# Kernel optimization log

Hardware: AMD Instinct MI355X
Metric: run time of the kernel (lower is better)

## Reference

```python
import jax, jax.numpy as jnp
import numpy as np

J, L = 4, 8
M = N = 128
B = 2
EPS = 1e-6  # abs_eps smoothing: |z|_eps = sqrt(re^2 + im^2 + eps)


def indices_third_order(J, L):
    # For each bandpass filter i = j1*L + l1, pair with every filter of scale
    # j2 >= j1 (all L angles) plus the lowpass (index J*L).
    # Count = J*L*(L*(J+1)/2 + 1) == num_coefficients.
    i_list, j_list = [], []
    for j1 in range(J):
        for l1 in range(L):
            i = j1 * L + l1
            for j2 in range(j1, J):
                for l2 in range(L):
                    i_list.append(i)
                    j_list.append(j2 * L + l2)
            i_list.append(i)
            j_list.append(J * L)
    return np.asarray(i_list), np.asarray(j_list)


def make_filters(J, L, M, N):
    # Real frequency-domain Morlet-like Gaussian bumps at J scales x L angles,
    # plus one lowpass. Shape (1, J*L+1, M, N), float32.
    kx = 2.0 * np.pi * np.fft.fftfreq(M)[:, None]
    ky = 2.0 * np.pi * np.fft.fftfreq(N)[None, :]
    filts = []
    for j in range(J):
        k0 = 0.8 * np.pi / 2.0 ** j
        sigma = 0.5 * k0
        for l in range(L):
            theta = np.pi * l / L
            cx, cy = k0 * np.cos(theta), k0 * np.sin(theta)
            filts.append(np.exp(-((kx - cx) ** 2 + (ky - cy) ** 2) / (2.0 * sigma ** 2)))
    sigma_lp = 0.8 * np.pi / 2.0 ** J
    filts.append(np.exp(-(kx ** 2 + ky ** 2) / (2.0 * sigma_lp ** 2)))
    return np.stack(filts)[None].astype(np.float32)


def abs_eps(z):
    return jnp.sqrt(z.real ** 2 + z.imag ** 2 + EPS)


def setup_inputs() -> dict:
    key = jax.random.key(0)
    x = jax.random.normal(key, (B, 1, M, N), dtype=jnp.float32)
    filters = jnp.asarray(make_filters(J, L, M, N))  # (1, 33, M, N)
    return {"x": x, "filters": filters}


def reference(x, filters):
    idx0, idx1 = indices_third_order(J, L)
    # first-order filtering: (B, nf, M, N) complex
    xf = jnp.fft.ifft2(filters * jnp.fft.fft2(x))
    xa = abs_eps(xf)  # real (B, nf, M, N)
    # cross-scale correlation: (B, nf_i, nf_j, M, N)
    inner = jnp.fft.ifft2(filters[:, None] * jnp.fft.fft2(xa)[:, :, None])
    out = jnp.real(jnp.conj(xf)[:, None] * inner).mean(axis=(-2, -1))  # (B, nf, nf)
    return out[:, idx0, idx1]  # (B, 672)
```

## Files before the change

kernel.cpp:

```cpp
#include <hip/hip_runtime.h>
#include <math.h>


#define PI_F 3.14159265358979323846f

__device__ __forceinline__ void make_tw(int lane, float* twr, float* twi) {
#pragma unroll
  for (int s = 0; s < 6; ++s) {
    int h = 32 >> s;
    float ang = -PI_F * (float)(lane & (h - 1)) / (float)h;
    float sv, cv;
    __sincosf(ang, &sv, &cv);
    twr[s] = cv; twi[s] = sv;
  }
  float ang = -PI_F * (float)lane / 64.0f;
  float sv, cv;
  __sincosf(ang, &sv, &cv);
  twr[6] = cv; twi[6] = sv;
}

template <int S>
__device__ __forceinline__ void fft128_dif(float& ar, float& ai, float& br, float& bi,
                                           const float* twr, const float* twi, int lane) {
  float s6r = twr[6], s6i = (S > 0) ? twi[6] : -twi[6];
  float ur = ar + br, ui = ai + bi;
  float vr = ar - br, vi = ai - bi;
  ar = ur; ai = ui;
  br = vr * s6r - vi * s6i;
  bi = vr * s6i + vi * s6r;
#pragma unroll
  for (int s = 0; s < 6; ++s) {
    int h = 32 >> s;
    float wr = twr[s], wi = (S > 0) ? twi[s] : -twi[s];
    bool hi = (lane & h) != 0;
    float pr, pi2;
    pr = __shfl_xor(ar, h, 64); pi2 = __shfl_xor(ai, h, 64);
    if (!hi) { ar += pr; ai += pi2; }
    else { float dr = pr - ar, di = pi2 - ai; ar = dr * wr - di * wi; ai = dr * wi + di * wr; }
    pr = __shfl_xor(br, h, 64); pi2 = __shfl_xor(bi, h, 64);
    if (!hi) { br += pr; bi += pi2; }
    else { float dr = pr - br, di = pi2 - bi; br = dr * wr - di * wi; bi = dr * wi + di * wr; }
  }
}

template <int NC>
__device__ __forceinline__ void transpose_r2c_n(float (&dr)[16], float (&di)[16],
    float (&er)[NC], float (&ei)[NC], float (&fr)[NC], float (&fi2)[NC],
    float2 (*tile)[128], int lane, int w, int colbase) {
#pragma unroll
  for (int ch = 0; ch < 2; ++ch) {
    if ((w >> 3) == ch) {
#pragma unroll
      for (int t = 0; t < 8; ++t) {
        int r = w * 8 + t;
        int rr = r & 63, sw = r & 15;
        tile[rr][lane ^ sw] = make_float2(dr[2 * t], di[2 * t]);
        tile[rr][(lane + 64) ^ sw] = make_float2(dr[2 * t + 1], di[2 * t + 1]);
      }
    }
    __syncthreads();
    {
      int sw = lane & 15;
#pragma unroll
      for (int ci = 0; ci < NC; ++ci) {
        int c = colbase + w * NC + ci;
        float2 v = tile[lane][c ^ sw];
        if (ch == 0) { er[ci] = v.x; ei[ci] = v.y; }
        else { fr[ci] = v.x; fi2[ci] = v.y; }
      }
    }
    __syncthreads();
  }
}

__global__ __launch_bounds__(1024, 2) void k_prep(const float* __restrict__ x,
    float2* __restrict__ X, float* __restrict__ out, const float* __restrict__ F,
    float* __restrict__ G) {
  __shared__ float2 tile[64][128];
  int tid = threadIdx.x;
  int bx = blockIdx.x;
  if (bx == 8) {
    if (tid < 1344) out[tid] = 0.f;
    return;
  }
  if (bx >= 9) {
    int j = bx - 9;
    const float* Fj = F + j * 16384;
    float* Gj = G + j * 16384;
    for (int k = tid; k < 16384; k += 1024) {
      int u = k >> 7, v = k & 127;
      int un = (128 - u) & 127, vn = (128 - v) & 127;
      float f = Fj[k], fn = Fj[un * 128 + vn];
      Gj[k] = 0.5f * (f * f + fn * fn);
    }
    return;
  }
  int b = bx >> 2, quarter = bx & 3;
  int lane = tid & 63, w = tid >> 6;
  float twr[7], twi[7]; make_tw(lane, twr, twi);
  const float* xb = x + b * 16384;
  float dr[16], di[16];
  float er[2], ei[2], fr[2], fi2[2];
#pragma unroll
  for (int t = 0; t < 8; ++t) {
    int r = w * 8 + t;
    float ar = xb[r * 128 + lane], ai2 = 0.f, br = xb[r * 128 + lane + 64], bi = 0.f;
    fft128_dif<1>(ar, ai2, br, bi, twr, twi, lane);
    dr[2 * t] = ar; di[2 * t] = ai2; dr[2 * t + 1] = br; di[2 * t + 1] = bi;
  }
  transpose_r2c_n<2>(dr, di, er, ei, fr, fi2, tile, lane, w, quarter * 32);
  int u0 = __brev((unsigned)lane) >> 25;
#pragma unroll
  for (int ci = 0; ci < 2; ++ci) {
    int c = quarter * 32 + w * 2 + ci;
    float ar = er[ci], ai2 = ei[ci], br = fr[ci], bi = fi2[ci];
    fft128_dif<1>(ar, ai2, br, bi, twr, twi, lane);
    int vn = __brev((unsigned)c) >> 25;
    X[b * 16384 + u0 * 128 + vn] = make_float2(ar, ai2);
    X[b * 16384 + (u0 + 1) * 128 + vn] = make_float2(br, bi);
  }
}

__global__ __launch_bounds__(1024, 2) void k_fields(const float2* __restrict__ X,
    const float* __restrict__ F, const float* __restrict__ G,
    float* __restrict__ dfld, float* __restrict__ xa) {
  __shared__ float2 tile[64][128];
  int tid = threadIdx.x, lane = tid & 63, w = tid >> 6;
  int bx = blockIdx.x;
  bool isd = (bx < 68);
  int b, half;
  bool has1 = false;
  const float* g0 = nullptr; const float* g1 = nullptr; const float* Fb = nullptr;
  float* o0; float* o1 = nullptr;
  if (isd) {
    int dp = bx >> 1; half = bx & 1;
    b = dp / 17; int p = dp - b * 17;
    int j0 = 2 * p; has1 = (p < 16);
    g0 = G + j0 * 16384;
    g1 = G + (j0 + 1) * 16384;
    o0 = dfld + (b * 33 + j0) * 16384;
    o1 = dfld + (b * 33 + j0 + 1) * 16384;
  } else {
    int q = bx - 68; int qi = q >> 1; half = q & 1;
    b = qi >> 5; int f = qi & 31;
    Fb = F + f * 16384;
    o0 = xa + qi * 16384;
  }
  float twr[7], twi[7]; make_tw(lane, twr, twi);
  const float2* Xb = X + b * 16384;
  float dr[16], di[16];
  float er[4], ei[4], fr[4], fi2[4];

#pragma unroll
  for (int t = 0; t < 8; ++t) {
    int r = w * 8 + t;
    float2 x0 = Xb[r * 128 + lane];
    float2 x1 = Xb[r * 128 + lane + 64];
    float ar, ai2, br, bi;
    if (isd) {
      float ga = g0[r * 128 + lane];
      float gb = has1 ? g1[r * 128 + lane] : 0.f;
      float gc = g0[r * 128 + lane + 64];
      float gd = has1 ? g1[r * 128 + lane + 64] : 0.f;
      ar = x0.x * ga - x0.y * gb; ai2 = x0.y * ga + x0.x * gb;
      br = x1.x * gc - x1.y * gd; bi = x1.y * gc + x1.x * gd;
    } else {
      float f0 = Fb[r * 128 + lane], f1 = Fb[r * 128 + lane + 64];
      ar = x0.x * f0; ai2 = x0.y * f0; br = x1.x * f1; bi = x1.y * f1;
    }
    fft128_dif<-1>(ar, ai2, br, bi, twr, twi, lane);
    dr[2 * t] = ar; di[2 * t] = ai2; dr[2 * t + 1] = br; di[2 * t + 1] = bi;
  }
  transpose_r2c_n<4>(dr, di, er, ei, fr, fi2, tile, lane, w, half * 64);

  const float sc = 1.0f / 16384.0f;
#pragma unroll
  for (int ci = 0; ci < 4; ++ci) {
    int c = half * 64 + w * 4 + ci;
    float ar = er[ci], ai2 = ei[ci], br = fr[ci], bi = fi2[ci];
    fft128_dif<-1>(ar, ai2, br, bi, twr, twi, lane);
    if (isd) {
      o0[c * 128 + lane] = ar;
      o0[c * 128 + lane + 64] = br;
      if (has1) {
        o1[c * 128 + lane] = ai2;
        o1[c * 128 + lane + 64] = bi;
      }
    } else {
      float t0r = ar * sc, t0i = ai2 * sc, t1r = br * sc, t1i = bi * sc;
      o0[c * 128 + lane] = sqrtf(t0r * t0r + t0i * t0i + 1e-6f);
      o0[c * 128 + lane + 64] = sqrtf(t1r * t1r + t1i * t1i + 1e-6f);
    }
  }
}

__global__ __launch_bounds__(512) void k_dot(const float* __restrict__ xa,
    const float* __restrict__ dfld, float* __restrict__ out) {
  int q = blockIdx.x;
  int im = q >> 3;
  int slice = (q >> 1) & 3;
  int jh = q & 1;
  int b = im >> 5, i = im & 31;
  int j0 = jh * 17;
  int t = threadIdx.x;
  const float4* xr = (const float4*)(xa + im * 16384 + slice * 4096);
  const float4* db = (const float4*)(dfld + (b * 33 + j0) * 16384 + slice * 4096);
  float acc[17];
#pragma unroll
  for (int j = 0; j < 17; ++j) acc[j] = 0.f;
#pragma unroll
  for (int it = 0; it < 2; ++it) {
    int k = it * 512 + t;
    float4 xv = xr[k];
#pragma unroll
    for (int j = 0; j < 17; ++j) {
      float4 dv = db[j * 4096 + k];
      acc[j] += xv.x * dv.x + xv.y * dv.y + xv.z * dv.z + xv.w * dv.w;
    }
  }
#pragma unroll
  for (int j = 0; j < 17; ++j) {
#pragma unroll
    for (int off = 32; off > 0; off >>= 1) acc[j] += __shfl_xor(acc[j], off, 64);
  }
  __shared__ float red[8][17];
  int w = t >> 6, lane = t & 63;
  if (lane == 0) {
#pragma unroll
    for (int j = 0; j < 17; ++j) red[w][j] = acc[j];
  }
  __syncthreads();
  if (t < 17) {
    int j = j0 + t;
    float s = 0.f;
#pragma unroll
    for (int w2 = 0; w2 < 8; ++w2) s += red[w2][t];
    int j1 = i >> 3, l1 = i & 7;
    const int pref[4] = {0, 264, 464, 600};
    int per = (4 - j1) * 8 + 1;
    int start = pref[j1] + l1 * per;
    int pos = -1;
    if (j == 32) pos = start + per - 1;
    else if (j < 32) {
      int j2 = j >> 3;
      if (j2 >= j1) pos = start + (j2 - j1) * 8 + (j & 7);
    }
    if (pos >= 0)
      atomicAdd(out + b * 672 + pos, s * (1.0f / 16384.0f) * (1.0f / 16384.0f));
  }
}

extern "C" void kernel_launch(void* const* d_in, const int* in_sizes, int n_in,
                              void* d_out, int out_size, void* d_ws, size_t ws_size,
                              hipStream_t stream) {
  (void)in_sizes; (void)n_in; (void)out_size; (void)ws_size;
  const float* x = (const float*)d_in[0];
  const float* F = (const float*)d_in[1];
  float* out = (float*)d_out;
  char* ws = (char*)d_ws;
  float2* X = (float2*)(ws + 0);
  float* dfld = (float*)(ws + 262144);
  float* xa = (float*)(ws + 4587520);
  float* G = (float*)(ws + 8781824);

  hipLaunchKernelGGL(k_prep, dim3(42), dim3(1024), 0, stream, x, X, out, F, G);
  hipLaunchKernelGGL(k_fields, dim3(196), dim3(1024), 0, stream, X, F, G, dfld, xa);
  hipLaunchKernelGGL(k_dot, dim3(512), dim3(512), 0, stream, xa, dfld, out);
}
```

Baseline: 103.3 us.

## Use half-wavefront 4-point FFT layout in k_fields and split G prep

Rewrites the k_fields 128-point FFTs so that each half-wavefront (32 lanes) handles one row with four elements per lane. The first two radix stages run in registers and only the remaining five use shuffles, which cuts cross-lane shuffle traffic and register-array size. The shared-memory transpose is rewritten to match the new layout and the launch bounds are relaxed to one block per SM. k_prep also splits the G-filter symmetrisation over four blocks per filter, raising the grid from 42 to 141 blocks for more parallelism.

```diff
diff --git a/kernel.cpp b/kernel.cpp
--- a/kernel.cpp
+++ b/kernel.cpp
@@ -73,6 +73,63 @@
   }
 }
 
+__device__ __forceinline__ void make_tw2(int q, float* t2r, float* t2i, float* hw) {
+#pragma unroll
+  for (int s = 0; s < 5; ++s) {
+    int h = 16 >> s;
+    float ang = -PI_F * (float)(q & (h - 1)) / (float)h;
+    float sv, cv;
+    __sincosf(ang, &sv, &cv);
+    t2r[s] = cv; t2i[s] = sv;
+  }
+  float sv, cv;
+  __sincosf(-PI_F * (float)q / 64.0f, &sv, &cv);         hw[0] = cv; hw[1] = sv;
+  __sincosf(-PI_F * (float)(q + 32) / 64.0f, &sv, &cv);  hw[2] = cv; hw[3] = sv;
+  __sincosf(-PI_F * (float)q / 32.0f, &sv, &cv);         hw[4] = cv; hw[5] = sv;
+}
+
+template <int S>
+__device__ __forceinline__ void fft128x2_dif(float (&cr)[4], float (&ci)[4],
+    const float* t2r, const float* t2i, const float* hw, int q) {
+  float T0r = hw[0], T0i = (S > 0) ? hw[1] : -hw[1];
+  float T1r = hw[2], T1i = (S > 0) ? hw[3] : -hw[3];
+  float T2r = hw[4], T2i = (S > 0) ? hw[5] : -hw[5];
+  {
+    float ur = cr[0] + cr[2], ui = ci[0] + ci[2];
+    float vr = cr[0] - cr[2], vi = ci[0] - ci[2];
+    cr[0] = ur; ci[0] = ui;
+    cr[2] = vr * T0r - vi * T0i; ci[2] = vr * T0i + vi * T0r;
+    ur = cr[1] + cr[3]; ui = ci[1] + ci[3];
+    vr = cr[1] - cr[3]; vi = ci[1] - ci[3];
+    cr[1] = ur; ci[1] = ui;
+    cr[3] = vr * T1r - vi * T1i; ci[3] = vr * T1i + vi * T1r;
+  }
+  {
+    float ur = cr[0] + cr[1], ui = ci[0] + ci[1];
+    float vr = cr[0] - cr[1], vi = ci[0] - ci[1];
+    cr[0] = ur; ci[0] = ui;
+    cr[1] = vr * T2r - vi * T2i; ci[1] = vr * T2i + vi * T2r;
+    ur = cr[2] + cr[3]; ui = ci[2] + ci[3];
+    vr = cr[2] - cr[3]; vi = ci[2] - ci[3];
+    cr[2] = ur; ci[2] = ui;
+    cr[3] = vr * T2r - vi * T2i; ci[3] = vr * T2i + vi * T2r;
+  }
+#pragma unroll
+  for (int s = 0; s < 5; ++s) {
+    int h = 16 >> s;
+    float wr = t2r[s], wi = (S > 0) ? t2i[s] : -t2i[s];
+    bool hi = (q & h) != 0;
+#pragma unroll
+    for (int m = 0; m < 4; ++m) {
+      float pr = __shfl_xor(cr[m], h, 64);
+      float pi2 = __shfl_xor(ci[m], h, 64);
+      if (!hi) { cr[m] += pr; ci[m] += pi2; }
+      else { float dr = pr - cr[m], di = pi2 - ci[m];
+             cr[m] = dr * wr - di * wi; ci[m] = dr * wi + di * wr; }
+    }
+  }
+}
+
 __global__ __launch_bounds__(1024, 2) void k_prep(const float* __restrict__ x,
     float2* __restrict__ X, float* __restrict__ out, const float* __restrict__ F,
     float* __restrict__ G) {
@@ -84,10 +141,13 @@
     return;
   }
   if (bx >= 9) {
-    int j = bx - 9;
+    int q = bx - 9;
+    int j = q >> 2, part = q & 3;
     const float* Fj = F + j * 16384;
     float* Gj = G + j * 16384;
-    for (int k = tid; k < 16384; k += 1024) {
+#pragma unroll
+    for (int it = 0; it < 4; ++it) {
+      int k = part * 4096 + it * 1024 + tid;
       int u = k >> 7, v = k & 127;
       int un = (128 - u) & 127, vn = (128 - v) & 127;
       float f = Fj[k], fn = Fj[un * 128 + vn];
@@ -121,11 +181,12 @@
   }
 }
 
-__global__ __launch_bounds__(1024, 2) void k_fields(const float2* __restrict__ X,
+__global__ __launch_bounds__(1024, 1) void k_fields(const float2* __restrict__ X,
     const float* __restrict__ F, const float* __restrict__ G,
     float* __restrict__ dfld, float* __restrict__ xa) {
   __shared__ float2 tile[64][128];
   int tid = threadIdx.x, lane = tid & 63, w = tid >> 6;
+  int g = lane >> 5, q = lane & 31;
   int bx = blockIdx.x;
   bool isd = (bx < 68);
   int b, half;
@@ -141,65 +202,93 @@
     o0 = dfld + (b * 33 + j0) * 16384;
     o1 = dfld + (b * 33 + j0 + 1) * 16384;
   } else {
-    int q = bx - 68; int qi = q >> 1; half = q & 1;
+    int qq = bx - 68; int qi = qq >> 1; half = qq & 1;
     b = qi >> 5; int f = qi & 31;
     Fb = F + f * 16384;
     o0 = xa + qi * 16384;
   }
-  float twr[7], twi[7]; make_tw(lane, twr, twi);
+  float t2r[5], t2i[5], hw[6];
+  make_tw2(q, t2r, t2i, hw);
   const float2* Xb = X + b * 16384;
-  float dr[16], di[16];
-  float er[4], ei[4], fr[4], fi2[4];
-
-#pragma unroll
-  for (int t = 0; t < 8; ++t) {
-    int r = w * 8 + t;
-    float2 x0 = Xb[r * 128 + lane];
-    float2 x1 = Xb[r * 128 + lane + 64];
-    float ar, ai2, br, bi;
-    if (isd) {
-      float ga = g0[r * 128 + lane];
-      float gb = has1 ? g1[r * 128 + lane] : 0.f;
-      float gc = g0[r * 128 + lane + 64];
-      float gd = has1 ? g1[r * 128 + lane + 64] : 0.f;
-      ar = x0.x * ga - x0.y * gb; ai2 = x0.y * ga + x0.x * gb;
-      br = x1.x * gc - x1.y * gd; bi = x1.y * gc + x1.x * gd;
-    } else {
-      float f0 = Fb[r * 128 + lane], f1 = Fb[r * 128 + lane + 64];
-      ar = x0.x * f0; ai2 = x0.y * f0; br = x1.x * f1; bi = x1.y * f1;
-    }
-    fft128_dif<-1>(ar, ai2, br, bi, twr, twi, lane);
-    dr[2 * t] = ar; di[2 * t] = ai2; dr[2 * t + 1] = br; di[2 * t + 1] = bi;
-  }
-  transpose_r2c_n<4>(dr, di, er, ei, fr, fi2, tile, lane, w, half * 64);
+
+  float sr[4][4], si[4][4];
+#pragma unroll
+  for (int k = 0; k < 4; ++k) {
+    int r = w * 8 + 2 * k + g;
+    float cr[4], ci[4];
+#pragma unroll
+    for (int m = 0; m < 4; ++m) {
+      int p = q + 32 * m;
+      float2 xv = Xb[r * 128 + p];
+      if (isd) {
+        float ga = g0[r * 128 + p];
+        float gb = has1 ? g1[r * 128 + p] : 0.f;
+        cr[m] = xv.x * ga - xv.y * gb; ci[m] = xv.y * ga + xv.x * gb;
+      } else {
+        float f0 = Fb[r * 128 + p];
+        cr[m] = xv.x * f0; ci[m] = xv.y * f0;
+      }
+    }
+    fft128x2_dif<-1>(cr, ci, t2r, t2i, hw, q);
+#pragma unroll
+    for (int m = 0; m < 4; ++m) { sr[k][m] = cr[m]; si[k][m] = ci[m]; }
+  }
+
+  float pr[2][4], pi2a[2][4];
+  int colbase = half * 64;
+#pragma unroll
+  for (int ch = 0; ch < 2; ++ch) {
+    if ((w >> 3) == ch) {
+#pragma unroll
+      for (int k = 0; k < 4; ++k) {
+        int r = w * 8 + 2 * k + g;
+        int rr = r & 63, sw = r & 15;
+#pragma unroll
+        for (int m = 0; m < 4; ++m)
+          tile[rr][(32 * m + q) ^ sw] = make_float2(sr[k][m], si[k][m]);
+      }
+    }
+    __syncthreads();
+    {
+      int sw = q & 15;
+#pragma unroll
+      for (int j = 0; j < 2; ++j) {
+        int c = colbase + w * 4 + 2 * j + g;
+#pragma unroll
+        for (int mm = 0; mm < 2; ++mm) {
+          float2 v = tile[32 * mm + q][c ^ sw];
+          pr[j][2 * ch + mm] = v.x; pi2a[j][2 * ch + mm] = v.y;
+        }
+      }
+    }
+    __syncthreads();
+  }
 
   const float sc = 1.0f / 16384.0f;
 #pragma unroll
-  for (int ci = 0; ci < 4; ++ci) {
-    int c = half * 64 + w * 4 + ci;
-    float ar = er[ci], ai2 = ei[ci], br = fr[ci], bi = fi2[ci];
-    fft128_dif<-1>(ar, ai2, br, bi, twr, twi, lane);
-    if (isd) {
-      o0[c * 128 + lane] = ar;
-      o0[c * 128 + lane + 64] = br;
-      if (has1) {
-        o1[c * 128 + lane] = ai2;
-        o1[c * 128 + lane + 64] = bi;
-      }
-    } else {
-      float t0r = ar * sc, t0i = ai2 * sc, t1r = br * sc, t1i = bi * sc;
-      o0[c * 128 + lane] = sqrtf(t0r * t0r + t0i * t0i + 1e-6f);
-      o0[c * 128 + lane + 64] = sqrtf(t1r * t1r + t1i * t1i + 1e-6f);
+  for (int j = 0; j < 2; ++j) {
+    fft128x2_dif<-1>(pr[j], pi2a[j], t2r, t2i, hw, q);
+    int c = colbase + w * 4 + 2 * j + g;
+#pragma unroll
+    for (int m = 0; m < 4; ++m) {
+      int su = 32 * m + q;
+      if (isd) {
+        o0[c * 128 + su] = pr[j][m];
+        if (has1) o1[c * 128 + su] = pi2a[j][m];
+      } else {
+        float tr = pr[j][m] * sc, ti = pi2a[j][m] * sc;
+        o0[c * 128 + su] = sqrtf(tr * tr + ti * ti + 1e-6f);
+      }
     }
   }
 }
 
 __global__ __launch_bounds__(512) void k_dot(const float* __restrict__ xa,
     const float* __restrict__ dfld, float* __restrict__ out) {
-  int q = blockIdx.x;
-  int im = q >> 3;
-  int slice = (q >> 1) & 3;
-  int jh = q & 1;
+  int qb = blockIdx.x;
+  int im = qb >> 3;
+  int slice = (qb >> 1) & 3;
+  int jh = qb & 1;
   int b = im >> 5, i = im & 31;
   int j0 = jh * 17;
   int t = threadIdx.x;
@@ -263,7 +352,7 @@
   float* xa = (float*)(ws + 4587520);
   float* G = (float*)(ws + 8781824);
 
-  hipLaunchKernelGGL(k_prep, dim3(42), dim3(1024), 0, stream, x, X, out, F, G);
+  hipLaunchKernelGGL(k_prep, dim3(141), dim3(1024), 0, stream, x, X, out, F, G);
   hipLaunchKernelGGL(k_fields, dim3(196), dim3(1024), 0, stream, X, F, G, dfld, xa);
   hipLaunchKernelGGL(k_dot, dim3(512), dim3(512), 0, stream, xa, dfld, out);
 }
```

New measurement: 103.5 us. Within noise of the previous version (+0.2%).
